# Optimization experiments

Hardware: AMD Instinct MI355X
Metric: run time of the kernel (lower is better)

## Reference

```python
import jax, jax.numpy as jnp
import numpy as np

H, W = 16, 16  # input_resolution
NUM_HEADS = 16
DIM = 512


def build_relative_position_index(h, w):
    coords = np.stack(np.meshgrid(np.arange(h), np.arange(w), indexing='ij'))  # [2,h,w]
    cf = coords.reshape(2, -1)
    rel = cf[:, :, None] - cf[:, None, :]            # [2,N,N]
    rel = rel.transpose(1, 2, 0).astype(np.int32)    # [N,N,2]
    rel[:, :, 0] += h - 1
    rel[:, :, 1] += w - 1
    rel[:, :, 0] *= 2 * w - 1
    return jnp.asarray(rel.sum(-1).reshape(-1), dtype=jnp.int32)  # [N*N]


def setup_inputs() -> dict:
    key = jax.random.key(0)
    ks = jax.random.split(key, 6)
    B, N, C = 128, H * W, DIM
    x = jax.random.normal(ks[0], (B, N, C), dtype=jnp.float32)
    qkv_w = jax.random.normal(ks[1], (3 * C, C), dtype=jnp.float32) * (C ** -0.5)
    qkv_b = jax.random.normal(ks[2], (3 * C,), dtype=jnp.float32) * 0.02
    proj_w = jax.random.normal(ks[3], (C, C), dtype=jnp.float32) * (C ** -0.5)
    proj_b = jax.random.normal(ks[4], (C,), dtype=jnp.float32) * 0.02
    bias_table = jax.random.normal(ks[5], ((2 * H - 1) * (2 * W - 1), NUM_HEADS), dtype=jnp.float32) * 0.02
    rel_index = build_relative_position_index(H, W)
    return {"x": x, "qkv_w": qkv_w, "qkv_b": qkv_b, "proj_w": proj_w,
            "proj_b": proj_b, "bias_table": bias_table, "rel_index": rel_index}


def reference(x, qkv_w, qkv_b, proj_w, proj_b, bias_table, rel_index):
    B, N, C = x.shape
    h = NUM_HEADS
    hd = C // h
    scale = hd ** -0.5
    # qkv projection: [B,N,3C] -> [3,B,h,N,hd]
    qkv = (jnp.einsum('bnc,oc->bno', x, qkv_w) + qkv_b)
    qkv = qkv.reshape(B, N, 3, h, hd).transpose(2, 0, 3, 1, 4)
    q, k, v = qkv[0], qkv[1], qkv[2]
    # relative position bias: gather [N*N,h] -> [1,h,N,N]
    bias = bias_table[rel_index].reshape(N, N, h).transpose(2, 0, 1)[None]
    attn = jnp.einsum('bhnd,bhmd->bhnm', q * scale, k) + bias
    attn = jax.nn.softmax(attn, axis=-1)
    out = jnp.einsum('bhnm,bhmd->bhnd', attn, v)     # [B,h,N,hd]
    out = out.transpose(0, 2, 1, 3).reshape(B, N, C)
    return jnp.einsum('bnc,oc->bno', out, proj_w) + proj_b
```

## Files before the change

kernel.cpp:

```cpp
#include <hip/hip_runtime.h>

typedef __bf16 bf16_t;
typedef __bf16 bf16x8 __attribute__((ext_vector_type(8)));
typedef float f32x4 __attribute__((ext_vector_type(4)));

#define MFMA_16x16x32(a, b, c) __builtin_amdgcn_mfma_f32_16x16x32_bf16((a), (b), (c), 0, 0, 0)

__device__ inline bf16x8 cvt8(const float* __restrict__ p) {
  bf16x8 r;
#pragma unroll
  for (int j = 0; j < 8; j++) r[j] = (bf16_t)p[j];
  return r;
}

__device__ inline void load_lds16(const bf16_t* g, bf16_t* l) {
  __builtin_amdgcn_global_load_lds(
      (const __attribute__((address_space(1))) void*)g,
      (__attribute__((address_space(3))) void*)l, 16, 0, 0);
}

__global__ __launch_bounds__(256) void prep_k(
    const float* __restrict__ x, const float* __restrict__ qkv_w,
    const float* __restrict__ proj_w, const float* __restrict__ table,
    const int* __restrict__ rel,
    bf16_t* __restrict__ xbf, bf16_t* __restrict__ wqkvbf,
    bf16_t* __restrict__ wprojbf, float* __restrict__ biasws) {
  const int bid = blockIdx.x;
  if (bid < 8704) {
    size_t base = ((size_t)bid * 256 + threadIdx.x) * 8;
    if (base < 16777216) {
      *(bf16x8*)(xbf + base) = cvt8(x + base);
    } else if (base < 17563648) {
      size_t o = base - 16777216;
      *(bf16x8*)(wqkvbf + o) = cvt8(qkv_w + o);
    } else {
      size_t o = base - 17563648;
      *(bf16x8*)(wprojbf + o) = cvt8(proj_w + o);
    }
  } else {
    int idx = (bid - 8704) * 256 + threadIdx.x;
    int h = idx >> 16;
    int rem = idx & 65535;
    int qb = rem >> 12;
    int ct = (rem >> 8) & 15;
    int L = (rem >> 2) & 63;
    int r = idx & 3;
    int q = qb * 16 + (L & 15);
    int k = ct * 16 + (L >> 4) * 4 + r;
    biasws[idx] = table[rel[q * 256 + k] * 16 + h];
  }
}

#define PH_OPEN() __builtin_amdgcn_s_setprio(1)

#define PH_CLOSE()                                        \
  do {                                                    \
    __builtin_amdgcn_s_setprio(0);                        \
    asm volatile("s_waitcnt lgkmcnt(0)" ::: "memory");    \
    __builtin_amdgcn_sched_barrier(0);                    \
    __builtin_amdgcn_s_barrier();                         \
    __builtin_amdgcn_sched_barrier(0);                    \
  } while (0)

#define GATE4()                                           \
  do {                                                    \
    __builtin_amdgcn_s_setprio(0);                        \
    asm volatile("s_waitcnt vmcnt(4)" ::: "memory");      \
    __builtin_amdgcn_s_barrier();                         \
    __builtin_amdgcn_sched_barrier(0);                    \
  } while (0)

#define GATE0()                                           \
  do {                                                    \
    __builtin_amdgcn_s_setprio(0);                        \
    asm volatile("s_waitcnt vmcnt(0)" ::: "memory");      \
    __builtin_amdgcn_s_barrier();                         \
    __builtin_amdgcn_sched_barrier(0);                    \
  } while (0)

#define STG2(src, dst, c)                                                        \
  do {                                                                           \
    load_lds16((src) + (c)*16384, (dst) + (c)*2048);                             \
    load_lds16((src) + ((c) + 1) * 16384, (dst) + ((c) + 1) * 2048);             \
  } while (0)

#define RDA2(dst, buf, ibase)                                                    \
  _Pragma("unroll") for (int i = 0; i < 2; ++i) {                                \
    dst[i][0] = *(const bf16x8*)&As[(buf)*8192 + a0 + ((ibase) + i) * 1024];     \
    dst[i][1] = *(const bf16x8*)&As[(buf)*8192 + a1 + ((ibase) + i) * 1024];     \
  }
#define RDB2(dst, buf, jbase)                                                    \
  _Pragma("unroll") for (int j = 0; j < 2; ++j) {                                \
    dst[j][0] = *(const bf16x8*)&Bs[(buf)*8192 + b0 + ((jbase) + j) * 1024];     \
    dst[j][1] = *(const bf16x8*)&Bs[(buf)*8192 + b1 + ((jbase) + j) * 1024];     \
  }

#define MFQ2(Af, Bf, I0, J0)                                                     \
  _Pragma("unroll") for (int i = 0; i < 2; ++i) _Pragma("unroll")                \
      for (int j = 0; j < 2; ++j) {                                              \
    acc[(I0) + i][(J0) + j] =                                                    \
        MFMA_16x16x32(Af[i][0], Bf[j][0], acc[(I0) + i][(J0) + j]);              \
    acc[(I0) + i][(J0) + j] =                                                    \
        MFMA_16x16x32(Af[i][1], Bf[j][1], acc[(I0) + i][(J0) + j]);              \
  }

#define GEMM_SETUP(Ap, Wp)                                                       \
  __shared__ bf16_t As[2 * 8192];                                                \
  __shared__ bf16_t Bs[2 * 8192];                                                \
  const int t = threadIdx.x;                                                     \
  const int w = t >> 6, L = t & 63;                                              \
  const int wm = w >> 1, wn = w & 1;                                             \
  const int lrow = L & 15, lq = L >> 4;                                          \
  const int srow = t >> 3;                                                       \
  const int sslot = (t & 7) ^ (srow & 7);                                        \
  const bf16_t* ga = (Ap) + (size_t)(m0 + srow) * 512 + sslot * 8;               \
  const bf16_t* gb = (Wp) + (size_t)(n0 + srow) * 512 + sslot * 8;               \
  bf16_t* la = As + t * 8;                                                       \
  bf16_t* lb = Bs + t * 8;                                                       \
  const int m8 = (lrow & 7) * 8;                                                 \
  const int a0 = (wm * 64 + lrow) * 64 + ((lq * 8) ^ m8);                        \
  const int a1 = (wm * 64 + lrow) * 64 + ((32 + lq * 8) ^ m8);                   \
  const int b0 = (wn * 64 + lrow) * 64 + ((lq * 8) ^ m8);                        \
  const int b1 = (wn * 64 + lrow) * 64 + ((32 + lq * 8) ^ m8);

#define PROLOGUE()                                                               \
  STG2(ga, la, 0); STG2(ga, la, 2);                                              \
  STG2(gb, lb, 0); STG2(gb, lb, 2);                                              \
  STG2(ga + 64, la + 8192, 0); STG2(ga + 64, la + 8192, 2);                      \
  asm volatile("s_waitcnt vmcnt(4)" ::: "memory");                               \
  __builtin_amdgcn_s_barrier();                                                  \
  __builtin_amdgcn_sched_barrier(0);

#define HALF_STEADY(CUR, LBDST, LADST, GBP, GAP)                                 \
  {                                                                              \
    bf16x8 fal[2][2], fbl[2][2], fah[2][2], fbh[2][2];                           \
    RDA2(fal, CUR, 0); RDB2(fbl, CUR, 0); RDB2(fbh, CUR, 2);                     \
    STG2(GBP, LBDST, 0);                                                         \
    PH_OPEN(); MFQ2(fal, fbl, 0, 0); PH_CLOSE();                                 \
    RDA2(fah, CUR, 2);                                                           \
    STG2(GBP, LBDST, 2);                                                         \
    PH_OPEN(); MFQ2(fal, fbh, 0, 2); PH_CLOSE();                                 \
    STG2(GAP, LADST, 0);                                                         \
    PH_OPEN(); MFQ2(fah, fbh, 2, 2); PH_CLOSE();                                 \
    STG2(GAP, LADST, 2);                                                         \
    PH_OPEN(); MFQ2(fah, fbl, 2, 0); GATE4();                                    \
  }

#define GEMM_LOOP()                                                              \
  {                                                                              \
    const bf16_t* gA = ga + 128;                                       \
    const bf16_t* gB = gb + 64;                                        \
    _Pragma("unroll 1") for (int G = 0; G < 3; ++G) {                            \
      HALF_STEADY(0, lb + 8192, la, gB, gA)                                      \
      HALF_STEADY(1, lb, la + 8192, gB + 64, gA + 64)                            \
      gA += 128; gB += 128;                                                      \
    }                                                                            \
    {            \
      bf16x8 fal[2][2], fbl[2][2], fah[2][2], fbh[2][2];                         \
      RDA2(fal, 0, 0); RDB2(fbl, 0, 0); RDB2(fbh, 0, 2);                         \
      STG2(gB, lb + 8192, 0);                                                    \
      PH_OPEN(); MFQ2(fal, fbl, 0, 0); PH_CLOSE();                               \
      RDA2(fah, 0, 2);                                                           \
      STG2(gB, lb + 8192, 2);                                                    \
      PH_OPEN(); MFQ2(fal, fbh, 0, 2); PH_CLOSE();                               \
      PH_OPEN(); MFQ2(fah, fbh, 2, 2); PH_CLOSE();                               \
      PH_OPEN(); MFQ2(fah, fbl, 2, 0); GATE0();                                  \
    }                                                                            \
    {                               \
      bf16x8 fal[2][2], fbl[2][2], fah[2][2], fbh[2][2];                         \
      RDA2(fal, 1, 0); RDB2(fbl, 1, 0); RDB2(fbh, 1, 2);                         \
      PH_OPEN(); MFQ2(fal, fbl, 0, 0); PH_CLOSE();                               \
      RDA2(fah, 1, 2);                                                           \
      PH_OPEN(); MFQ2(fal, fbh, 0, 2); PH_CLOSE();                               \
      PH_OPEN(); MFQ2(fah, fbh, 2, 2); PH_CLOSE();                               \
      PH_OPEN(); MFQ2(fah, fbl, 2, 0);                                           \
      __builtin_amdgcn_s_setprio(0);                                             \
      __builtin_amdgcn_sched_barrier(0);                                         \
    }                                                                            \
  }

__global__ __launch_bounds__(256, 2) void qkv_gemm128_k(
    const bf16_t* __restrict__ A, const bf16_t* __restrict__ W,
    const float* __restrict__ Bvec,
    bf16_t* __restrict__ qws, bf16_t* __restrict__ kws, bf16_t* __restrict__ vws) {
  const int id = blockIdx.x;
  const int wg = (id & 7) * 384 + (id >> 3);
  const int mt = wg / 12, nt = wg % 12;
  const int m0 = mt * 128, n0 = nt * 128;

  GEMM_SETUP(A, W);

  f32x4 acc[4][4];
#pragma unroll
  for (int jj = 0; jj < 4; ++jj) {
    float bv = Bvec[n0 + wn * 64 + jj * 16 + lrow];
#pragma unroll
    for (int i = 0; i < 4; ++i) acc[i][jj] = (f32x4){bv, bv, bv, bv};
  }

  PROLOGUE();
  GEMM_LOOP();

  const int col0 = n0 + wn * 64;
  const int s = col0 >> 9;
  bf16_t* dst = (s == 0) ? qws : (s == 1) ? kws : vws;
  const float mul = (s == 0) ? 0.17677669529663687f : 1.0f;
#pragma unroll
  for (int jj = 0; jj < 4; ++jj) {
    int o = col0 + jj * 16 + lrow;
    int rem = o & 511;
    int hh = rem >> 5, d = rem & 31;
#pragma unroll
    for (int i = 0; i < 4; ++i) {
#pragma unroll
      for (int r = 0; r < 4; ++r) {
        int m = m0 + wm * 64 + i * 16 + lq * 4 + r;
        int b = m >> 8, n = m & 255;
        dst[(size_t)(((b * 16 + hh) * 256 + n) << 5) + d] =
            (bf16_t)(acc[i][jj][r] * mul);
      }
    }
  }
}

__global__ __launch_bounds__(256, 2) void proj_gemm128_k(
    const bf16_t* __restrict__ A, const bf16_t* __restrict__ W,
    const float* __restrict__ Bvec, float* __restrict__ out) {
  const int id = blockIdx.x;
  const int wg = (id & 7) * 128 + (id >> 3);
  const int mt = wg >> 2, nt = wg & 3;
  const int m0 = mt * 128, n0 = nt * 128;

  GEMM_SETUP(A, W);

  f32x4 acc[4][4];
#pragma unroll
  for (int jj = 0; jj < 4; ++jj) {
    float bv = Bvec[n0 + wn * 64 + jj * 16 + lrow];
#pragma unroll
    for (int i = 0; i < 4; ++i) acc[i][jj] = (f32x4){bv, bv, bv, bv};
  }

  PROLOGUE();
  GEMM_LOOP();

#pragma unroll
  for (int jj = 0; jj < 4; ++jj) {
    int o = n0 + wn * 64 + jj * 16 + lrow;
#pragma unroll
    for (int i = 0; i < 4; ++i) {
#pragma unroll
      for (int r = 0; r < 4; ++r) {
        int m = m0 + wm * 64 + i * 16 + lq * 4 + r;
        out[(size_t)m * 512 + o] = acc[i][jj][r];
      }
    }
  }
}

__global__ __launch_bounds__(256) void attn_k(
    const bf16_t* __restrict__ qws, const bf16_t* __restrict__ kws,
    const bf16_t* __restrict__ vws, const float* __restrict__ biasws,
    bf16_t* __restrict__ aows) {
  __shared__ __align__(16) bf16_t Vs[32 * 264];

  const int id = blockIdx.x;
  const int xcd = id & 7;
  const int jj = id >> 3;
  const int bh = (jj >> 2) * 8 + xcd;
  const int strip = jj & 3;
  const int h = bh & 15, b = bh >> 4;

  const int t = threadIdx.x;
  const int w = t >> 6, L = t & 63;
  const int lrow = L & 15, lq = L >> 4;

  const bf16_t* kbase = kws + (size_t)bh * 8192;
  const bf16_t* vbase = vws + (size_t)bh * 8192;

#pragma unroll
  for (int c = 0; c < 4; c++) {
    bf16x8 vv = *(const bf16x8*)(vbase + t * 32 + c * 8);
#pragma unroll
    for (int j = 0; j < 8; j++) Vs[(c * 8 + j) * 264 + t] = vv[j];
  }
  __syncthreads();

  const int idxA = ((2 * (lq & 1)) * 16 + lrow) * 4;
  const int idxB = idxA + 64;
  const bool gsel = (lq < 2);

  const int qrow0 = strip * 64 + w * 16;
  const bf16_t* qbase = qws + (size_t)bh * 8192 + qrow0 * 32;
  bf16x8 qf = *(const bf16x8*)(qbase + lrow * 32 + lq * 8);
  const float* bb = biasws + h * 65536 + (strip * 4 + w) * 4096;

  f32x4 S[16];
#pragma unroll
  for (int ct = 0; ct < 16; ct++) {
    bf16x8 kf = *(const bf16x8*)(kbase + (ct * 16 + lrow) * 32 + lq * 8);
    f32x4 bi = *(const f32x4*)(bb + ct * 256 + L * 4);
    S[ct] = MFMA_16x16x32(kf, qf, bi);
  }

  f32x4 sv = {};
#pragma unroll
  for (int ct = 0; ct < 16; ct++) {
#pragma unroll
    for (int r = 0; r < 4; r++) S[ct][r] = __expf(S[ct][r]);
    sv += S[ct];
  }
  float sm = (sv[0] + sv[1]) + (sv[2] + sv[3]);
  sm += __shfl_xor(sm, 16, 64);
  sm += __shfl_xor(sm, 32, 64);
  const float inv = 1.0f / sm;

  int pd[16][2];
#pragma unroll
  for (int ct = 0; ct < 16; ct++) {
#pragma unroll
    for (int j = 0; j < 2; j++) {
      float lo = S[ct][2 * j] * inv;
      float hi = S[ct][2 * j + 1] * inv;
      int d;
      asm("v_cvt_pk_bf16_f32 %0, %1, %2" : "=v"(d) : "v"(lo), "v"(hi));
      pd[ct][j] = d;
    }
  }

  f32x4 O0 = {}, O1 = {};
#pragma unroll
  for (int kt = 0; kt < 8; kt++) {
    int rA0 = __builtin_amdgcn_ds_bpermute(idxA, pd[2 * kt][0]);
    int rA1 = __builtin_amdgcn_ds_bpermute(idxA, pd[2 * kt][1]);
    int rA2 = __builtin_amdgcn_ds_bpermute(idxB, pd[2 * kt][0]);
    int rA3 = __builtin_amdgcn_ds_bpermute(idxB, pd[2 * kt][1]);
    int rB0 = __builtin_amdgcn_ds_bpermute(idxA, pd[2 * kt + 1][0]);
    int rB1 = __builtin_amdgcn_ds_bpermute(idxA, pd[2 * kt + 1][1]);
    int rB2 = __builtin_amdgcn_ds_bpermute(idxB, pd[2 * kt + 1][0]);
    int rB3 = __builtin_amdgcn_ds_bpermute(idxB, pd[2 * kt + 1][1]);
    int4 Di;
    Di.x = gsel ? rA0 : rB0;
    Di.y = gsel ? rA1 : rB1;
    Di.z = gsel ? rA2 : rB2;
    Di.w = gsel ? rA3 : rB3;
    bf16x8 pf = *reinterpret_cast<bf16x8*>(&Di);
    bf16x8 v0 = *(const bf16x8*)&Vs[lrow * 264 + kt * 32 + lq * 8];
    bf16x8 v1 = *(const bf16x8*)&Vs[(16 + lrow) * 264 + kt * 32 + lq * 8];
    O0 = MFMA_16x16x32(pf, v0, O0);
    O1 = MFMA_16x16x32(pf, v1, O1);
  }

  bf16_t* obase = aows + (size_t)(b * 256 + qrow0) * 512 + h * 32;
#pragma unroll
  for (int r = 0; r < 4; r++) {
    int rl = lq * 4 + r;
    obase[rl * 512 + lrow] = (bf16_t)(O0[r]);
    obase[rl * 512 + 16 + lrow] = (bf16_t)(O1[r]);
  }
}

extern "C" void kernel_launch(void* const* d_in, const int* in_sizes, int n_in,
                              void* d_out, int out_size, void* d_ws, size_t ws_size,
                              hipStream_t stream) {
  (void)in_sizes; (void)n_in; (void)out_size; (void)ws_size;
  const float* x      = (const float*)d_in[0];
  const float* qkv_w  = (const float*)d_in[1];
  const float* qkv_b  = (const float*)d_in[2];
  const float* proj_w = (const float*)d_in[3];
  const float* proj_b = (const float*)d_in[4];
  const float* table  = (const float*)d_in[5];
  const int*   rel    = (const int*)d_in[6];

  const size_t QKV_ELEMS = 16777216;
  bf16_t* qws     = (bf16_t*)d_ws;
  bf16_t* kws     = qws + QKV_ELEMS;
  bf16_t* vws     = kws + QKV_ELEMS;
  float*  biasws  = (float*)(vws + QKV_ELEMS);
  bf16_t* wqkvbf  = (bf16_t*)(biasws + 1048576);
  bf16_t* wprojbf = wqkvbf + 786432;
  bf16_t* xbf     = wprojbf + 262144;
  bf16_t* aows    = xbf;
  float*  out     = (float*)d_out;

  prep_k<<<12800, 256, 0, stream>>>(x, qkv_w, proj_w, table, rel,
                                    xbf, wqkvbf, wprojbf, biasws);
  qkv_gemm128_k<<<3072, 256, 0, stream>>>(xbf, wqkvbf, qkv_b, qws, kws, vws);
  attn_k<<<8192, 256, 0, stream>>>(qws, kws, vws, biasws, aows);
  proj_gemm128_k<<<1024, 256, 0, stream>>>(aows, wprojbf, proj_b, out);
}
```

Measured before the change: 302.7 us.

## Stage softmax probabilities through LDS instead of bpermute shuffles in attention

Swaps the QK^T MFMA operand order so each lane holds query rows, and reorders the precomputed bias layout to match. Unnormalized exp scores are written to a per-wave LDS tile and read back as the A operand for PV, which removes the ds_bpermute register shuffles. Normalization is deferred to the output, and all K fragments are loaded up front. The cost is more LDS (about 50KB per block, which may reduce occupancy), scattered 2-byte LDS stores, and a 16-lane shuffle reduction per row instead of two shuffles.

```diff
diff --git a/kernel.cpp b/kernel.cpp
--- a/kernel.cpp
+++ b/kernel.cpp
@@ -41,13 +41,13 @@
     int idx = (bid - 8704) * 256 + threadIdx.x;
     int h = idx >> 16;
     int rem = idx & 65535;
-    int qb = rem >> 12;
+    int rb = rem >> 12;
     int ct = (rem >> 8) & 15;
     int L = (rem >> 2) & 63;
     int r = idx & 3;
-    int q = qb * 16 + (L & 15);
-    int k = ct * 16 + (L >> 4) * 4 + r;
-    biasws[idx] = table[rel[q * 256 + k] * 16 + h];
+    int row = rb * 16 + (L >> 4) * 4 + r;
+    int col = ct * 16 + (L & 15);
+    biasws[idx] = table[rel[row * 256 + col] * 16 + h];
   }
 }
 
@@ -262,7 +262,9 @@
     const bf16_t* __restrict__ qws, const bf16_t* __restrict__ kws,
     const bf16_t* __restrict__ vws, const float* __restrict__ biasws,
     bf16_t* __restrict__ aows) {
-  __shared__ __align__(16) bf16_t Vs[32 * 264];
+  __shared__ __align__(16) char smem[33792 + 16896];
+  bf16_t* Ps = (bf16_t*)smem;
+  bf16_t* Vs = (bf16_t*)(smem + 33792);
 
   const int id = blockIdx.x;
   const int xcd = id & 7;
@@ -277,86 +279,70 @@
 
   const bf16_t* kbase = kws + (size_t)bh * 8192;
   const bf16_t* vbase = vws + (size_t)bh * 8192;
-
 #pragma unroll
   for (int c = 0; c < 4; c++) {
     bf16x8 vv = *(const bf16x8*)(vbase + t * 32 + c * 8);
 #pragma unroll
     for (int j = 0; j < 8; j++) Vs[(c * 8 + j) * 264 + t] = vv[j];
   }
+
+  const bf16_t* qbase = qws + (size_t)bh * 8192 + (strip * 64 + w * 16) * 32;
+  bf16x8 qf = *(const bf16x8*)(qbase + lrow * 32 + lq * 8);
+  bf16x8 kf[16];
+#pragma unroll
+  for (int ct = 0; ct < 16; ct++)
+    kf[ct] = *(const bf16x8*)(kbase + (ct * 16 + lrow) * 32 + lq * 8);
+
+  const float* bb = biasws + h * 65536 + (strip * 4 + w) * 4096;
+  f32x4 S[16];
+#pragma unroll
+  for (int ct = 0; ct < 16; ct++) {
+    f32x4 bi = *(const f32x4*)(bb + ct * 256 + L * 4);
+    S[ct] = MFMA_16x16x32(qf, kf[ct], bi);
+  }
+
+  float sm[4] = {0.f, 0.f, 0.f, 0.f};
+#pragma unroll
+  for (int ct = 0; ct < 16; ct++)
+#pragma unroll
+    for (int r = 0; r < 4; r++) {
+      float e = __expf(S[ct][r]);
+      S[ct][r] = e;
+      sm[r] += e;
+    }
+#pragma unroll
+  for (int r = 0; r < 4; r++)
+#pragma unroll
+    for (int msk = 1; msk < 16; msk <<= 1)
+      sm[r] += __shfl_xor(sm[r], msk, 64);
+  float inv[4];
+#pragma unroll
+  for (int r = 0; r < 4; r++) inv[r] = 1.0f / sm[r];
+
+  bf16_t* Pw = Ps + w * 4224;
+#pragma unroll
+  for (int ct = 0; ct < 16; ct++)
+#pragma unroll
+    for (int r = 0; r < 4; r++)
+      Pw[(lq * 4 + r) * 264 + ct * 16 + lrow] = (bf16_t)S[ct][r];
+
   __syncthreads();
 
-  const int idxA = ((2 * (lq & 1)) * 16 + lrow) * 4;
-  const int idxB = idxA + 64;
-  const bool gsel = (lq < 2);
-
-  const int qrow0 = strip * 64 + w * 16;
-  const bf16_t* qbase = qws + (size_t)bh * 8192 + qrow0 * 32;
-  bf16x8 qf = *(const bf16x8*)(qbase + lrow * 32 + lq * 8);
-  const float* bb = biasws + h * 65536 + (strip * 4 + w) * 4096;
-
-  f32x4 S[16];
-#pragma unroll
-  for (int ct = 0; ct < 16; ct++) {
-    bf16x8 kf = *(const bf16x8*)(kbase + (ct * 16 + lrow) * 32 + lq * 8);
-    f32x4 bi = *(const f32x4*)(bb + ct * 256 + L * 4);
-    S[ct] = MFMA_16x16x32(kf, qf, bi);
-  }
-
-  f32x4 sv = {};
-#pragma unroll
-  for (int ct = 0; ct < 16; ct++) {
-#pragma unroll
-    for (int r = 0; r < 4; r++) S[ct][r] = __expf(S[ct][r]);
-    sv += S[ct];
-  }
-  float sm = (sv[0] + sv[1]) + (sv[2] + sv[3]);
-  sm += __shfl_xor(sm, 16, 64);
-  sm += __shfl_xor(sm, 32, 64);
-  const float inv = 1.0f / sm;
-
-  int pd[16][2];
-#pragma unroll
-  for (int ct = 0; ct < 16; ct++) {
-#pragma unroll
-    for (int j = 0; j < 2; j++) {
-      float lo = S[ct][2 * j] * inv;
-      float hi = S[ct][2 * j + 1] * inv;
-      int d;
-      asm("v_cvt_pk_bf16_f32 %0, %1, %2" : "=v"(d) : "v"(lo), "v"(hi));
-      pd[ct][j] = d;
-    }
-  }
-
   f32x4 O0 = {}, O1 = {};
 #pragma unroll
-  for (int kt = 0; kt < 8; kt++) {
-    int rA0 = __builtin_amdgcn_ds_bpermute(idxA, pd[2 * kt][0]);
-    int rA1 = __builtin_amdgcn_ds_bpermute(idxA, pd[2 * kt][1]);
-    int rA2 = __builtin_amdgcn_ds_bpermute(idxB, pd[2 * kt][0]);
-    int rA3 = __builtin_amdgcn_ds_bpermute(idxB, pd[2 * kt][1]);
-    int rB0 = __builtin_amdgcn_ds_bpermute(idxA, pd[2 * kt + 1][0]);
-    int rB1 = __builtin_amdgcn_ds_bpermute(idxA, pd[2 * kt + 1][1]);
-    int rB2 = __builtin_amdgcn_ds_bpermute(idxB, pd[2 * kt + 1][0]);
-    int rB3 = __builtin_amdgcn_ds_bpermute(idxB, pd[2 * kt + 1][1]);
-    int4 Di;
-    Di.x = gsel ? rA0 : rB0;
-    Di.y = gsel ? rA1 : rB1;
-    Di.z = gsel ? rA2 : rB2;
-    Di.w = gsel ? rA3 : rB3;
-    bf16x8 pf = *reinterpret_cast<bf16x8*>(&Di);
-    bf16x8 v0 = *(const bf16x8*)&Vs[lrow * 264 + kt * 32 + lq * 8];
-    bf16x8 v1 = *(const bf16x8*)&Vs[(16 + lrow) * 264 + kt * 32 + lq * 8];
+  for (int c = 0; c < 8; c++) {
+    bf16x8 pf = *(const bf16x8*)&Pw[lrow * 264 + c * 32 + lq * 8];
+    bf16x8 v0 = *(const bf16x8*)&Vs[lrow * 264 + c * 32 + lq * 8];
+    bf16x8 v1 = *(const bf16x8*)&Vs[(16 + lrow) * 264 + c * 32 + lq * 8];
     O0 = MFMA_16x16x32(pf, v0, O0);
     O1 = MFMA_16x16x32(pf, v1, O1);
   }
-
-  bf16_t* obase = aows + (size_t)(b * 256 + qrow0) * 512 + h * 32;
+  bf16_t* obase = aows + (size_t)(b * 256 + strip * 64 + w * 16) * 512 + h * 32;
 #pragma unroll
   for (int r = 0; r < 4; r++) {
     int rl = lq * 4 + r;
-    obase[rl * 512 + lrow] = (bf16_t)(O0[r]);
-    obase[rl * 512 + 16 + lrow] = (bf16_t)(O1[r]);
+    obase[rl * 512 + lrow] = (bf16_t)(O0[r] * inv[r]);
+    obase[rl * 512 + 16 + lrow] = (bf16_t)(O1[r] * inv[r]);
   }
 }
 
```

After: 279.4 us. -7.7%, faster.
